# Optimization experiments

Measured on AMD Instinct MI355X. Metric: run time of the kernel, lower is better.

The kernel has to match this reference:

```python
import jax, jax.numpy as jnp
import numpy as np

N_NODES = 100000
N_EDGES = 3200000
NFEAT, NHID, NCLASS = 512, 256, 40


def spmm(edge_src, edge_dst, edge_w, h):
    # sparse adjacency @ h via gather + weighted segment-sum over destination nodes
    msgs = h[edge_src] * edge_w[:, None]          # [E, d]
    return jax.ops.segment_sum(msgs, edge_dst, num_segments=N_NODES)


def gcn_layer(h, W, b, edge_src, edge_dst, edge_w):
    support = h @ W                                # [N, d_out]
    return spmm(edge_src, edge_dst, edge_w, support) + b


def setup_inputs() -> dict:
    key = jax.random.key(0)
    ks = jax.random.split(key, 16)
    def w(k, shape, fan_in):
        return jax.random.normal(k, shape, dtype=jnp.float32) / np.sqrt(fan_in)
    inp = {
        'x': jax.random.normal(ks[0], (N_NODES, NFEAT), dtype=jnp.float32),
        'W1': w(ks[1], (NFEAT, NHID), NFEAT), 'b1': jnp.zeros((NHID,), jnp.float32),
        'W2': w(ks[2], (NHID, NHID), NHID),  'b2': jnp.zeros((NHID,), jnp.float32),
        'W3': w(ks[3], (NHID, NHID), NHID),  'b3': jnp.zeros((NHID,), jnp.float32),
        'W4': w(ks[4], (NHID, NHID), NHID),  'b4': jnp.zeros((NHID,), jnp.float32),
        'W5': w(ks[5], (NHID, NHID), NHID),  'b5': jnp.zeros((NHID,), jnp.float32),
        'W6': w(ks[6], (NHID, NCLASS), NHID),'b6': jnp.zeros((NCLASS,), jnp.float32),
        'edge_w': jax.random.uniform(ks[7], (N_EDGES,), dtype=jnp.float32),
        'edge_src': jax.random.randint(ks[8], (N_EDGES,), 0, N_NODES, dtype=jnp.int32),
        'edge_dst': jax.random.randint(ks[9], (N_EDGES,), 0, N_NODES, dtype=jnp.int32),
    }
    return inp


def reference(x, W1, b1, W2, b2, W3, b3, W4, b4, W5, b5, W6, b6,
              edge_w, edge_src, edge_dst):
    # eval mode: dropout is identity
    h = jax.nn.relu(gcn_layer(x, W1, b1, edge_src, edge_dst, edge_w))
    h = jax.nn.relu(gcn_layer(h, W2, b2, edge_src, edge_dst, edge_w))
    h = jax.nn.relu(gcn_layer(h, W3, b3, edge_src, edge_dst, edge_w))
    h = jax.nn.relu(gcn_layer(h, W4, b4, edge_src, edge_dst, edge_w))
    h = jax.nn.relu(gcn_layer(h, W5, b5, edge_src, edge_dst, edge_w))
    h = gcn_layer(h, W6, b6, edge_src, edge_dst, edge_w)
    return jax.nn.log_softmax(h, axis=1)
```

## Files before the change

### kernel.cpp

```cpp
#include <hip/hip_runtime.h>
#include <hip/hip_bf16.h>

static const int NN = 100000;
static const int NE = 3200000;
static const int F0 = 512;
static const int FH = 256;
static const int NC = 40;

#define CHUNK_SHIFT 13
static const int NCH  = (NN + (1 << CHUNK_SHIFT) - 1) >> CHUNK_SHIFT;
static const int KEYS = NN * NCH;

#define NPB_SHIFT 8
static const int NPB = 1 << NPB_SHIFT;
static const int NB  = (NN + NPB - 1) >> NPB_SHIFT;
static const int KPB = NPB * NCH;
#define EPB_A 8192

typedef __attribute__((ext_vector_type(8))) short bf16x8;
typedef __attribute__((ext_vector_type(16))) float f32x16;

__device__ __forceinline__ float bf2f(unsigned short u) {
    union { unsigned int i; float f; } c; c.i = ((unsigned int)u) << 16; return c.f;
}
__device__ __forceinline__ unsigned short f2bf(float f) {
    __hip_bfloat16 h = __float2bfloat16(f);
    return *reinterpret_cast<unsigned short*>(&h);
}

__global__ __launch_bounds__(256) void hist_bucket(const int* __restrict__ dst,
                                                   int* __restrict__ bcount, int E) {
    __shared__ int h[NB];
    for (int i = threadIdx.x; i < NB; i += 256) h[i] = 0;
    __syncthreads();
    for (int e = blockIdx.x * 256 + threadIdx.x; e < E; e += gridDim.x * 256)
        atomicAdd(&h[dst[e] >> NPB_SHIFT], 1);
    __syncthreads();
    for (int i = threadIdx.x; i < NB; i += 256)
        if (h[i]) atomicAdd(&bcount[i], h[i]);
}

__global__ __launch_bounds__(512) void scan_buckets(const int* __restrict__ bcount,
                                                    int* __restrict__ bstart,
                                                    int* __restrict__ bcursor, int E) {
    __shared__ int t[512];
    int tid = threadIdx.x;
    int v = (tid < NB) ? bcount[tid] : 0;
    t[tid] = v;
    __syncthreads();
    for (int off = 1; off < 512; off <<= 1) {
        int u = (tid >= off) ? t[tid - off] : 0;
        __syncthreads();
        t[tid] += u;
        __syncthreads();
    }
    if (tid < NB) {
        int s = t[tid] - v;
        bstart[tid] = s;
        bcursor[tid] = s;
    }
    if (tid == 0) bstart[NB] = E;
}

__global__ __launch_bounds__(256) void bin_scatter(const int* __restrict__ src,
                                                   const int* __restrict__ dst,
                                                   const float* __restrict__ w,
                                                   int* __restrict__ bcursor,
                                                   uint2* __restrict__ binned, int E) {
    __shared__ int hist[NB];
    __shared__ int base[NB];
    int tid = threadIdx.x;
    int e0 = blockIdx.x * EPB_A;
    int e1 = e0 + EPB_A; if (e1 > E) e1 = E;
    for (int i = tid; i < NB; i += 256) hist[i] = 0;
    __syncthreads();
    for (int e = e0 + tid; e < e1; e += 256)
        atomicAdd(&hist[dst[e] >> NPB_SHIFT], 1);
    __syncthreads();
    for (int i = tid; i < NB; i += 256) {
        int c = hist[i];
        base[i] = c ? atomicAdd(&bcursor[i], c) : 0;
        hist[i] = 0;
    }
    __syncthreads();
    for (int e = e0 + tid; e < e1; e += 256) {
        int d = dst[e];
        int b = d >> NPB_SHIFT;
        int off = atomicAdd(&hist[b], 1);
        unsigned int wq = (unsigned int)rintf(w[e] * 32767.f);
        unsigned int packed = ((unsigned int)src[e] << 15) | wq;
        binned[base[b] + off] = make_uint2(packed, (unsigned int)d);
    }
}

__global__ __launch_bounds__(256) void bin_sort(const uint2* __restrict__ binned,
                                                const int* __restrict__ bstart,
                                                int* __restrict__ keyStart,
                                                unsigned int* __restrict__ ev, int E) {
    __shared__ int hist[KPB];
    __shared__ int part[256];
    int b = blockIdx.x;
    int tid = threadIdx.x;
    int nodeLo = b << NPB_SHIFT;
    int eLo = bstart[b], eHi = bstart[b + 1];

    for (int i = tid; i < KPB; i += 256) hist[i] = 0;
    __syncthreads();
    for (int e = eLo + tid; e < eHi; e += 256) {
        uint2 r = binned[e];
        int lkey = ((int)r.y - nodeLo) * NCH + (int)(r.x >> (15 + CHUNK_SHIFT));
        atomicAdd(&hist[lkey], 1);
    }
    __syncthreads();

    int k0 = tid * NCH;
    int loc[NCH];
    int s = 0;
    #pragma unroll
    for (int j = 0; j < NCH; j++) { int c = hist[k0 + j]; loc[j] = s; s += c; }
    part[tid] = s;
    __syncthreads();
    for (int off = 1; off < 256; off <<= 1) {
        int u = (tid >= off) ? part[tid - off] : 0;
        __syncthreads();
        part[tid] += u;
        __syncthreads();
    }
    int excl = (tid > 0) ? part[tid - 1] : 0;
    __syncthreads();
    #pragma unroll
    for (int j = 0; j < NCH; j++) hist[k0 + j] = loc[j] + excl;
    __syncthreads();

    int keyBase = nodeLo * NCH;
    int kMax = KEYS - keyBase; if (kMax > KPB) kMax = KPB;
    for (int i = tid; i < kMax; i += 256) keyStart[keyBase + i] = eLo + hist[i];
    if (b == gridDim.x - 1 && tid == 0) keyStart[KEYS] = E;
    __syncthreads();

    for (int e = eLo + tid; e < eHi; e += 256) {
        uint2 r = binned[e];
        int lkey = ((int)r.y - nodeLo) * NCH + (int)(r.x >> (15 + CHUNK_SHIFT));
        int pos = eLo + atomicAdd(&hist[lkey], 1);
        ev[pos] = r.x;
    }
}

__global__ void transpose_cast(const float* __restrict__ W, unsigned short* __restrict__ Wt,
                               int K, int N) {
    int idx = blockIdx.x * 256 + threadIdx.x;
    if (idx >= K * N) return;
    int n = idx / K;
    int k = idx - n * K;
    Wt[idx] = f2bf(W[(size_t)k * N + n]);
}

template <int A_IS_F32>
__global__ __launch_bounds__(512, 2) void gemm_mfma_q(const void* __restrict__ Aptr,
                                                      const unsigned short* __restrict__ Wt,
                                                      unsigned char* __restrict__ Cq,
                                                      float* __restrict__ scales,
                                                      int M, int K) {
    __shared__ short Bs[65536];
    const int tid = threadIdx.x;
    const int w = tid >> 6;
    const int l = tid & 63;
    const int m0 = blockIdx.x * 256 + w * 32;
    const int lrow = l & 31;
    const int lgrp = l >> 5;
    int row_a = m0 + lrow;
    if (row_a > M - 1) row_a = M - 1;

    f32x16 acc[8] = {};

    for (int kt = 0; kt < K; kt += 256) {
        if (kt) __syncthreads();
        #pragma unroll
        for (int it = 0; it < 16; ++it) {
            int fid = it * 512 + tid;
            int c = fid & 255;
            int f = fid >> 8;
            bf16x8 v = *reinterpret_cast<const bf16x8*>(Wt + (size_t)c * K + kt + f * 8);
            *reinterpret_cast<bf16x8*>(&Bs[((f << 8) + c) * 8]) = v;
        }
        __syncthreads();

        for (int kk = 0; kk < 256; kk += 32) {
            bf16x8 a0, a1;
            if (A_IS_F32) {
                const float* p0 = (const float*)Aptr + (size_t)row_a * K + kt + kk + lgrp * 8;
                const float* p1 = p0 + 16;
                #pragma unroll
                for (int j = 0; j < 8; j++) a0[j] = (short)f2bf(p0[j]);
                #pragma unroll
                for (int j = 0; j < 8; j++) a1[j] = (short)f2bf(p1[j]);
            } else {
                const unsigned short* p = (const unsigned short*)Aptr + (size_t)row_a * K + kt + kk + lgrp * 8;
                a0 = *reinterpret_cast<const bf16x8*>(p);
                a1 = *reinterpret_cast<const bf16x8*>(p + 16);
            }
            const int fbase = kk >> 3;
            #pragma unroll
            for (int s = 0; s < 2; s++) {
                const short* bp = &Bs[((fbase + s * 2 + lgrp) << 8) * 8];
                bf16x8 a = s ? a1 : a0;
                #pragma unroll
                for (int nt = 0; nt < 8; nt++) {
                    bf16x8 b = *reinterpret_cast<const bf16x8*>(bp + (nt * 32 + lrow) * 8);
                    acc[nt] = __builtin_amdgcn_mfma_f32_32x32x16_bf16(a, b, acc[nt], 0, 0, 0);
                }
            }
        }
    }

    #pragma unroll
    for (int r = 0; r < 16; r++) {
        float vm = 0.f;
        #pragma unroll
        for (int nt = 0; nt < 8; nt++) vm = fmaxf(vm, fabsf(acc[nt][r]));
        #pragma unroll
        for (int off = 1; off < 32; off <<= 1) vm = fmaxf(vm, __shfl_xor(vm, off));
        int row = m0 + (r & 3) + 8 * (r >> 2) + 4 * lgrp;
        float inv = (vm > 0.f) ? 127.f / vm : 0.f;
        if (row < M) {
            if (lrow == 0) scales[row] = vm * (1.f / 127.f);
            #pragma unroll
            for (int nt = 0; nt < 8; nt++) {
                int q = (int)rintf(acc[nt][r] * inv) + 128;
                Cq[(size_t)row * 256 + nt * 32 + lrow] = (unsigned char)q;
            }
        }
    }
}

__global__ __launch_bounds__(256) void spmm_kernel(const unsigned char* __restrict__ supq,
                                                   const float* __restrict__ scales,
                                                   const unsigned int* __restrict__ ev,
                                                   const int* __restrict__ keyStart,
                                                   const float* __restrict__ bias,
                                                   unsigned short* __restrict__ out,
                                                   int M, int do_relu) {
    int node = blockIdx.x * 4 + (threadIdx.x >> 6);
    int l = threadIdx.x & 63;
    if (node >= M) return;
    const int g = l >> 4;
    const int lane16 = l & 15;
    const int boff = lane16 * 16;
    const int kb = node * NCH;
    int e0 = keyStart[kb], e1 = keyStart[kb + NCH];

    float acc[16] = {};
    float sw = 0.f;
    int e = e0 + g;
    for (; e + 4 < e1; e += 8) {
        unsigned int m0 = ev[e], m1 = ev[e + 4];
        int s0 = m0 >> 15, s1 = m1 >> 15;
        float w0 = (float)(m0 & 0x7fffu) * scales[s0];
        float w1 = (float)(m1 & 0x7fffu) * scales[s1];
        uint4 r0 = *(const uint4*)(supq + (size_t)s0 * 256 + boff);
        uint4 r1 = *(const uint4*)(supq + (size_t)s1 * 256 + boff);
        sw += w0 + w1;
        const unsigned int rr0[4] = {r0.x, r0.y, r0.z, r0.w};
        const unsigned int rr1[4] = {r1.x, r1.y, r1.z, r1.w};
        #pragma unroll
        for (int q = 0; q < 4; q++) {
            #pragma unroll
            for (int j = 0; j < 4; j++) {
                acc[q * 4 + j] += w0 * (float)((rr0[q] >> (8 * j)) & 0xffu)
                                + w1 * (float)((rr1[q] >> (8 * j)) & 0xffu);
            }
        }
    }
    for (; e < e1; e += 4) {
        unsigned int m0 = ev[e];
        int s0 = m0 >> 15;
        float w0 = (float)(m0 & 0x7fffu) * scales[s0];
        uint4 r0 = *(const uint4*)(supq + (size_t)s0 * 256 + boff);
        sw += w0;
        const unsigned int rr0[4] = {r0.x, r0.y, r0.z, r0.w};
        #pragma unroll
        for (int q = 0; q < 4; q++) {
            #pragma unroll
            for (int j = 0; j < 4; j++)
                acc[q * 4 + j] += w0 * (float)((rr0[q] >> (8 * j)) & 0xffu);
        }
    }

    #pragma unroll
    for (int j = 0; j < 16; j++) {
        acc[j] += __shfl_xor(acc[j], 16);
        acc[j] += __shfl_xor(acc[j], 32);
    }
    sw += __shfl_xor(sw, 16);
    sw += __shfl_xor(sw, 32);

    if (g == 0) {
        const float* bp = bias + boff;
        bf16x8 o0, o1;
        #pragma unroll
        for (int j = 0; j < 8; j++) {
            float v = (acc[j] - 128.f * sw) * (1.f / 32767.f) + bp[j];
            if (do_relu) v = fmaxf(v, 0.f);
            o0[j] = (short)f2bf(v);
        }
        #pragma unroll
        for (int j = 0; j < 8; j++) {
            float v = (acc[8 + j] - 128.f * sw) * (1.f / 32767.f) + bp[8 + j];
            if (do_relu) v = fmaxf(v, 0.f);
            o1[j] = (short)f2bf(v);
        }
        *reinterpret_cast<bf16x8*>(out + (size_t)node * 256 + boff) = o0;
        *reinterpret_cast<bf16x8*>(out + (size_t)node * 256 + boff + 8) = o1;
    }
}

__global__ __launch_bounds__(256) void gemm6_mfma(const unsigned short* __restrict__ h,
                                                  const unsigned short* __restrict__ Wt6,
                                                  unsigned short* __restrict__ sup6, int M) {
    __shared__ short Bs[64][40];
    const int tid = threadIdx.x;
    const int w = tid >> 6;
    const int l = tid & 63;
    const int m0 = blockIdx.x * 128 + w * 32;
    const int lrow = l & 31;
    const int lgrp = l >> 5;
    int row_a = m0 + lrow;
    if (row_a > M - 1) row_a = M - 1;

    f32x16 acc[2] = {};

    for (int kk = 0; kk < 256; kk += 32) {
        __syncthreads();
        {
            int r = tid >> 2, part = tid & 3;
            bf16x8 v = {};
            if (r < NC) v = *(const bf16x8*)(Wt6 + (size_t)r * 256 + kk + part * 8);
            *reinterpret_cast<bf16x8*>(&Bs[r][part * 8]) = v;
        }
        __syncthreads();

        #pragma unroll
        for (int s = 0; s < 2; s++) {
            const unsigned short* pa = h + (size_t)row_a * 256 + kk + s * 16 + lgrp * 8;
            bf16x8 a = *(const bf16x8*)pa;
            #pragma unroll
            for (int nt = 0; nt < 2; nt++) {
                bf16x8 b = *(const bf16x8*)(&Bs[nt * 32 + lrow][s * 16 + lgrp * 8]);
                acc[nt] = __builtin_amdgcn_mfma_f32_32x32x16_bf16(a, b, acc[nt], 0, 0, 0);
            }
        }
    }

    #pragma unroll
    for (int nt = 0; nt < 2; nt++) {
        #pragma unroll
        for (int r = 0; r < 16; r++) {
            int row = m0 + (r & 3) + 8 * (r >> 2) + 4 * lgrp;
            int col = nt * 32 + lrow;
            if (row < M && col < NC) sup6[(size_t)row * NC + col] = f2bf(acc[nt][r]);
        }
    }
}

__global__ __launch_bounds__(256) void spmm6_lsm(const unsigned short* __restrict__ sup6,
                                                 const unsigned int* __restrict__ ev,
                                                 const int* __restrict__ keyStart,
                                                 const float* __restrict__ b6,
                                                 float* __restrict__ out, int M) {
    int node = blockIdx.x * 4 + (threadIdx.x >> 6);
    int l = threadIdx.x & 63;
    if (node >= M) return;
    const int kb = node * NCH;
    int e0 = keyStart[kb], e1 = keyStart[kb + NCH];
    float acc = 0.f;
    bool active = (l < NC);
    int cix = active ? l : 0;
    int e = e0;
    for (; e + 4 <= e1; e += 4) {
        unsigned int m0 = ev[e], m1 = ev[e + 1], m2 = ev[e + 2], m3 = ev[e + 3];
        float v0 = bf2f(sup6[(size_t)(m0 >> 15) * NC + cix]);
        float v1 = bf2f(sup6[(size_t)(m1 >> 15) * NC + cix]);
        float v2 = bf2f(sup6[(size_t)(m2 >> 15) * NC + cix]);
        float v3 = bf2f(sup6[(size_t)(m3 >> 15) * NC + cix]);
        acc += (float)(m0 & 0x7fffu) * v0 + (float)(m1 & 0x7fffu) * v1
             + (float)(m2 & 0x7fffu) * v2 + (float)(m3 & 0x7fffu) * v3;
    }
    for (; e < e1; e++) {
        unsigned int m0 = ev[e];
        acc += (float)(m0 & 0x7fffu) * bf2f(sup6[(size_t)(m0 >> 15) * NC + cix]);
    }
    acc *= (1.f / 32767.f);

    float x = active ? (acc + b6[l]) : -__builtin_inff();
    float mx = x;
    #pragma unroll
    for (int off = 32; off > 0; off >>= 1) mx = fmaxf(mx, __shfl_xor(mx, off));
    float ex = active ? __expf(x - mx) : 0.f;
    float sm = ex;
    #pragma unroll
    for (int off = 32; off > 0; off >>= 1) sm += __shfl_xor(sm, off);
    if (active) out[(size_t)node * NC + l] = x - mx - __logf(sm);
}

extern "C" void kernel_launch(void* const* d_in, const int* in_sizes, int n_in,
                              void* d_out, int out_size, void* d_ws, size_t ws_size,
                              hipStream_t stream) {
    const float* x  = (const float*)d_in[0];
    const float* W1 = (const float*)d_in[1];  const float* b1 = (const float*)d_in[2];
    const float* W2 = (const float*)d_in[3];  const float* b2 = (const float*)d_in[4];
    const float* W3 = (const float*)d_in[5];  const float* b3 = (const float*)d_in[6];
    const float* W4 = (const float*)d_in[7];  const float* b4 = (const float*)d_in[8];
    const float* W5 = (const float*)d_in[9];  const float* b5 = (const float*)d_in[10];
    const float* W6 = (const float*)d_in[11]; const float* b6 = (const float*)d_in[12];
    const float* edge_w  = (const float*)d_in[13];
    const int* edge_src  = (const int*)d_in[14];
    const int* edge_dst  = (const int*)d_in[15];

    char* p = (char*)d_ws;
    auto alloc = [&](size_t bytes) -> char* {
        char* r = p;
        p += (bytes + 255) & ~(size_t)255;
        return r;
    };
    unsigned short* h_a = (unsigned short*)alloc((size_t)NN * FH * 2);
    unsigned short* h_b = (unsigned short*)alloc((size_t)NN * FH * 2);
    unsigned char* supq = (unsigned char*)alloc((size_t)NN * 256);
    float* scales       = (float*)alloc((size_t)NN * 4);
    unsigned int* ev    = (unsigned int*)alloc((size_t)NE * 4);
    int* keyStart  = (int*)alloc((size_t)(KEYS + 1) * 4);
    int* bcount    = (int*)alloc((size_t)NB * 4);
    int* bstart    = (int*)alloc((size_t)(NB + 1) * 4);
    int* bcursor   = (int*)alloc((size_t)NB * 4);
    unsigned short* Wt1 = (unsigned short*)alloc((size_t)FH * F0 * 2);
    unsigned short* Wt2 = (unsigned short*)alloc((size_t)FH * FH * 2);
    unsigned short* Wt3 = (unsigned short*)alloc((size_t)FH * FH * 2);
    unsigned short* Wt4 = (unsigned short*)alloc((size_t)FH * FH * 2);
    unsigned short* Wt5 = (unsigned short*)alloc((size_t)FH * FH * 2);
    unsigned short* Wt6 = (unsigned short*)alloc((size_t)NC * FH * 2);
    unsigned short* sup6 = h_b;
    uint2* binned = (uint2*)h_b;

    hipMemsetAsync(bcount, 0, (size_t)NB * 4, stream);
    hist_bucket<<<512, 256, 0, stream>>>(edge_dst, bcount, NE);
    scan_buckets<<<1, 512, 0, stream>>>(bcount, bstart, bcursor, NE);
    bin_scatter<<<(NE + EPB_A - 1) / EPB_A, 256, 0, stream>>>(edge_src, edge_dst, edge_w,
                                                              bcursor, binned, NE);
    bin_sort<<<NB, 256, 0, stream>>>(binned, bstart, keyStart, ev, NE);

    transpose_cast<<<(F0 * FH + 255) / 256, 256, 0, stream>>>(W1, Wt1, F0, FH);
    transpose_cast<<<(FH * FH + 255) / 256, 256, 0, stream>>>(W2, Wt2, FH, FH);
    transpose_cast<<<(FH * FH + 255) / 256, 256, 0, stream>>>(W3, Wt3, FH, FH);
    transpose_cast<<<(FH * FH + 255) / 256, 256, 0, stream>>>(W4, Wt4, FH, FH);
    transpose_cast<<<(FH * FH + 255) / 256, 256, 0, stream>>>(W5, Wt5, FH, FH);
    transpose_cast<<<(FH * NC + 255) / 256, 256, 0, stream>>>(W6, Wt6, FH, NC);

    const int gemmGrid = (NN + 255) / 256;
    const int g6Grid   = (NN + 127) / 128;
    const int rowGrid  = (NN + 3) / 4;

    gemm_mfma_q<1><<<gemmGrid, 512, 0, stream>>>(x, Wt1, supq, scales, NN, F0);
    spmm_kernel<<<rowGrid, 256, 0, stream>>>(supq, scales, ev, keyStart, b1, h_a, NN, 1);
    gemm_mfma_q<0><<<gemmGrid, 512, 0, stream>>>(h_a, Wt2, supq, scales, NN, FH);
    spmm_kernel<<<rowGrid, 256, 0, stream>>>(supq, scales, ev, keyStart, b2, h_b, NN, 1);
    gemm_mfma_q<0><<<gemmGrid, 512, 0, stream>>>(h_b, Wt3, supq, scales, NN, FH);
    spmm_kernel<<<rowGrid, 256, 0, stream>>>(supq, scales, ev, keyStart, b3, h_a, NN, 1);
    gemm_mfma_q<0><<<gemmGrid, 512, 0, stream>>>(h_a, Wt4, supq, scales, NN, FH);
    spmm_kernel<<<rowGrid, 256, 0, stream>>>(supq, scales, ev, keyStart, b4, h_b, NN, 1);
    gemm_mfma_q<0><<<gemmGrid, 512, 0, stream>>>(h_b, Wt5, supq, scales, NN, FH);
    spmm_kernel<<<rowGrid, 256, 0, stream>>>(supq, scales, ev, keyStart, b5, h_a, NN, 1);
    gemm6_mfma<<<g6Grid, 256, 0, stream>>>(h_a, Wt6, sup6, NN);
    spmm6_lsm<<<rowGrid, 256, 0, stream>>>(sup6, ev, keyStart, b6, (float*)d_out, NN);
}
```

Before: 1.152 ms.

## Software-pipeline edge gathers in SpMM with multi-stage register prefetch

The SpMM inner loop now uses a three-stage register pipeline. Edge metadata is loaded three iterations ahead, and the quantized feature rows and scales are gathered two iterations ahead, so that memory latency overlaps with the FMA accumulation. The separate tail loop is dropped in favor of predicated loads that substitute zeros when out of range. This keeps more gathers in flight per wave, at the cost of extra registers that could lower occupancy.

New measurement: 1.181 ms. 1.03x slower.

```diff
diff --git a/kernel.cpp b/kernel.cpp
--- a/kernel.cpp
+++ b/kernel.cpp
@@ -251,17 +251,41 @@
 
     float acc[16] = {};
     float sw = 0.f;
-    int e = e0 + g;
-    for (; e + 4 < e1; e += 8) {
-        unsigned int m0 = ev[e], m1 = ev[e + 4];
-        int s0 = m0 >> 15, s1 = m1 >> 15;
-        float w0 = (float)(m0 & 0x7fffu) * scales[s0];
-        float w1 = (float)(m1 & 0x7fffu) * scales[s1];
-        uint4 r0 = *(const uint4*)(supq + (size_t)s0 * 256 + boff);
-        uint4 r1 = *(const uint4*)(supq + (size_t)s1 * 256 + boff);
+
+    int eP = e0 + g;
+
+    unsigned int mA0 = 0, mB0 = 0, mA1 = 0, mB1 = 0, mA2 = 0, mB2 = 0;
+    float sA0 = 0.f, sB0 = 0.f, sA1 = 0.f, sB1 = 0.f;
+    uint4 z4 = make_uint4(0, 0, 0, 0);
+    uint4 rA0 = z4, rB0 = z4, rA1 = z4, rB1 = z4;
+    bool vA0 = eP < e1,      vB0 = eP + 4 < e1;
+    bool vA1 = eP + 8 < e1,  vB1 = eP + 12 < e1;
+    bool vA2 = eP + 16 < e1, vB2 = eP + 20 < e1;
+    if (vA0) mA0 = ev[eP];
+    if (vB0) mB0 = ev[eP + 4];
+    if (vA1) mA1 = ev[eP + 8];
+    if (vB1) mB1 = ev[eP + 12];
+    if (vA2) mA2 = ev[eP + 16];
+    if (vB2) mB2 = ev[eP + 20];
+    if (vA0) { int s = mA0 >> 15; sA0 = scales[s]; rA0 = *(const uint4*)(supq + (size_t)s * 256 + boff); }
+    if (vB0) { int s = mB0 >> 15; sB0 = scales[s]; rB0 = *(const uint4*)(supq + (size_t)s * 256 + boff); }
+    if (vA1) { int s = mA1 >> 15; sA1 = scales[s]; rA1 = *(const uint4*)(supq + (size_t)s * 256 + boff); }
+    if (vB1) { int s = mB1 >> 15; sB1 = scales[s]; rB1 = *(const uint4*)(supq + (size_t)s * 256 + boff); }
+
+    while (vA0) {
+        float sA2 = 0.f, sB2 = 0.f;
+        uint4 rA2 = z4, rB2 = z4;
+        if (vA2) { int s = mA2 >> 15; sA2 = scales[s]; rA2 = *(const uint4*)(supq + (size_t)s * 256 + boff); }
+        if (vB2) { int s = mB2 >> 15; sB2 = scales[s]; rB2 = *(const uint4*)(supq + (size_t)s * 256 + boff); }
+        bool vA3 = eP + 24 < e1, vB3 = eP + 28 < e1;
+        unsigned int mA3 = 0, mB3 = 0;
+        if (vA3) mA3 = ev[eP + 24];
+        if (vB3) mB3 = ev[eP + 28];
+        float w0 = (float)(mA0 & 0x7fffu) * sA0;
+        float w1 = (float)(mB0 & 0x7fffu) * sB0;
         sw += w0 + w1;
-        const unsigned int rr0[4] = {r0.x, r0.y, r0.z, r0.w};
-        const unsigned int rr1[4] = {r1.x, r1.y, r1.z, r1.w};
+        const unsigned int rr0[4] = {rA0.x, rA0.y, rA0.z, rA0.w};
+        const unsigned int rr1[4] = {rB0.x, rB0.y, rB0.z, rB0.w};
         #pragma unroll
         for (int q = 0; q < 4; q++) {
             #pragma unroll
@@ -270,20 +294,10 @@
                                 + w1 * (float)((rr1[q] >> (8 * j)) & 0xffu);
             }
         }
-    }
-    for (; e < e1; e += 4) {
-        unsigned int m0 = ev[e];
-        int s0 = m0 >> 15;
-        float w0 = (float)(m0 & 0x7fffu) * scales[s0];
-        uint4 r0 = *(const uint4*)(supq + (size_t)s0 * 256 + boff);
-        sw += w0;
-        const unsigned int rr0[4] = {r0.x, r0.y, r0.z, r0.w};
-        #pragma unroll
-        for (int q = 0; q < 4; q++) {
-            #pragma unroll
-            for (int j = 0; j < 4; j++)
-                acc[q * 4 + j] += w0 * (float)((rr0[q] >> (8 * j)) & 0xffu);
-        }
+        mA0 = mA1; mB0 = mB1; sA0 = sA1; sB0 = sB1; rA0 = rA1; rB0 = rB1; vA0 = vA1; vB0 = vB1;
+        mA1 = mA2; mB1 = mB2; sA1 = sA2; sB1 = sB2; rA1 = rA2; rB1 = rB2; vA1 = vA2; vB1 = vB2;
+        mA2 = mA3; mB2 = mB3; vA2 = vA3; vB2 = vB3;
+        eP += 8;
     }
 
     #pragma unroll
```
